# Performance work log

Measured on AMD Instinct MI355X. Metric: run time of the kernel, lower is better.

The kernel has to match this reference:

```python
import jax, jax.numpy as jnp
import numpy as np

B, T, D, H, C, M = 128, 96, 256, 256, 8, 64
COMB = 4 * D + H  # z, z_prime, x_i, global_dynamics, h


def setup_inputs() -> dict:
    key = jax.random.key(0)
    ks = jax.random.split(key, 24)
    X = jax.random.normal(ks[0], (B, T, D), jnp.float32)
    X_last = jax.random.normal(ks[1], (B, T, D), jnp.float32)
    Mask = jax.random.bernoulli(ks[2], 0.5, (B, T, D)).astype(jnp.float32)
    Delta = jax.random.uniform(ks[3], (B, T, D), jnp.float32, 0.0, 5.0)
    X_last_b = jax.random.normal(ks[4], (B, T, D), jnp.float32)
    Delta_b = jax.random.uniform(ks[5], (B, T, D), jnp.float32, 0.0, 5.0)
    x = jnp.stack([X, X_last, Mask, Delta, X_last_b, Delta_b], axis=1)  # [B,6,T,D]
    X_mean = jax.random.normal(ks[6], (1, T, D), jnp.float32)
    clusters = jax.random.randint(ks[7], (D,), 1, C + 1, jnp.int64)
    s = 1.0 / np.sqrt(COMB)
    def U(k, shape, sc):
        return jax.random.uniform(k, shape, jnp.float32, -sc, sc)
    params = {
        'W_i': U(ks[8], (H, COMB), s), 'b_i': U(ks[9], (H,), s),
        'W_f': U(ks[10], (H, COMB), s), 'b_f': U(ks[11], (H,), s),
        'W_o': U(ks[12], (H, COMB), s), 'b_o': U(ks[13], (H,), s),
        'W_c': U(ks[14], (H, COMB), s), 'b_c': U(ks[15], (H,), s),
        'W_fc': U(ks[16], (D, H), 1.0 / np.sqrt(H)), 'b_fc': U(ks[17], (D,), 1.0 / np.sqrt(H)),
        'gz_w': U(ks[18], (D,), 1.0 / np.sqrt(D)), 'gz_b': U(ks[19], (D,), 1.0 / np.sqrt(D)),
        'gzp_w': U(ks[20], (D,), 1.0 / np.sqrt(D)), 'gzp_b': U(ks[21], (D,), 1.0 / np.sqrt(D)),
        'memory': jax.random.uniform(ks[22], (C, M, D), jnp.float32, -1.0 / np.sqrt(M), 1.0 / np.sqrt(M)),
    }
    k2 = jax.random.split(ks[23], 2)
    params['local_w'] = jax.random.uniform(k2[0], (3, D), jnp.float32, -1.0 / np.sqrt(3.0), 1.0 / np.sqrt(3.0))
    params['global_w'] = jax.random.uniform(k2[1], (C,), jnp.float32, -1.0 / np.sqrt(C), 1.0 / np.sqrt(C))
    return dict(x=x, X_mean=X_mean, clusters=clusters, **params)


def reference(x, X_mean, clusters, W_i, b_i, W_f, b_f, W_o, b_o, W_c, b_c,
              W_fc, b_fc, gz_w, gz_b, gzp_w, gzp_b, memory, local_w, global_w):
    # cluster one-hot feature masks: [C, D] (cluster ids are 1-based)
    cmask = (clusters[None, :] == jnp.arange(1, C + 1, dtype=clusters.dtype)[:, None]).astype(x.dtype)

    X, X_last, Mask, Delta, X_last_b, Delta_b = [x[:, i] for i in range(6)]  # each [B,T,D]
    xm = X_mean[0]  # [T,D]

    def step(carry, inp):
        h, c = carry
        xt, xl, xlb, m, d, db, mean = inp
        # FilterLinear with eye filter == diagonal linear; GRU-D decay
        dz = jnp.exp(-jax.nn.relu(d * gz_w + gz_b))
        dzp = jnp.exp(-jax.nn.relu(db * gzp_w + gzp_b))
        z = m * xt + (1 - m) * (dz * xl + (1 - dz) * mean)
        zp = m * xt + (1 - m) * (dzp * xlb + (1 - dzp) * mean)
        x_i = h @ W_fc.T + b_fc  # [B,D]
        local_stats = local_w[0] * z + local_w[1] * zp + local_w[2] * x_i  # [B,D]
        # per-cluster masked local stats -> memory attention
        li = local_stats[:, None, :] * cmask[None]              # [B,C,D]
        scores = jnp.einsum('cmd,bcd->bcm', memory, li)          # [B,C,M]
        s = jax.nn.softmax(scores, axis=-1)
        gd = jnp.einsum('bcm,cmd->bcd', s, memory)               # [B,C,D]
        gd = jnp.einsum('bcd,c->bd', gd, global_w)               # [B,D]
        combined = jnp.concatenate([z, zp, x_i, gd, h], axis=1)  # [B,4D+H]
        i = jax.nn.sigmoid(combined @ W_i.T + b_i)
        f = jax.nn.sigmoid(combined @ W_f.T + b_f)
        o = jax.nn.sigmoid(combined @ W_o.T + b_o)
        ct = jnp.tanh(combined @ W_c.T + b_c)
        c = f * c + i * ct
        h = o * jnp.tanh(c)
        out = h @ W_fc.T + b_fc
        return (h, c), out

    h0 = jnp.zeros((x.shape[0], H), x.dtype)
    c0 = jnp.zeros((x.shape[0], H), x.dtype)
    xs = (X.transpose(1, 0, 2), X_last.transpose(1, 0, 2), X_last_b.transpose(1, 0, 2),
          Mask.transpose(1, 0, 2), Delta.transpose(1, 0, 2), Delta_b.transpose(1, 0, 2), xm)
    _, outs = jax.lax.scan(step, (h0, c0), xs)
    return outs.transpose(1, 0, 2)  # [B,T,D]
```

## Files before the change

### kernel.cpp

```cpp
#include <hip/hip_runtime.h>
#include <hip/hip_bf16.h>
#include <hip/hip_fp16.h>
#include <cstdint>
#include <cstddef>


#define PLANE 24576

using bf16_t = __hip_bfloat16;
typedef __bf16 bf16x8 __attribute__((ext_vector_type(8)));
typedef float  f32x4  __attribute__((ext_vector_type(4)));
typedef unsigned int u32x4 __attribute__((ext_vector_type(4)));

__device__ __forceinline__ float  b2f(bf16_t v){ return __bfloat162float(v); }
__device__ __forceinline__ bf16_t f2b(float v){ return __float2bfloat16(v); }
__device__ __forceinline__ float ldF(const void* p, size_t i, int f32){
  return f32 ? ((const float*)p)[i] : b2f(((const bf16_t*)p)[i]);
}
__device__ __forceinline__ bf16x8 ld_frag(const void* p){
  union { uint4 u; bf16x8 v; } c;
  c.u = *(const uint4*)p;
  return c.v;
}
__device__ __forceinline__ f32x4 mfma_bf16(bf16x8 a, bf16x8 b, f32x4 c){
  return __builtin_amdgcn_mfma_f32_16x16x32_bf16(a, b, c, 0, 0, 0);
}

__device__ __forceinline__ u32x4 ld_cg(const void* p){
  u32x4 r;
  asm volatile("global_load_dwordx4 %0, %1, off sc0 sc1"
               : "=v"(r) : "v"(p) : "memory");
  return r;
}
__device__ __forceinline__ void st_cg(void* p, u32x4 v){
  asm volatile("global_store_dwordx4 %0, %1, off sc0 sc1"
               :: "v"(p), "v"(v) : "memory");
}
__device__ __forceinline__ void st_flag(int* p, int v){
  asm volatile("global_store_dword %0, %1, off sc0 sc1"
               :: "v"(p), "v"(v) : "memory");
}
__device__ __forceinline__ int ld_flag(const int* p){
  int r;
  asm volatile("global_load_dword %0, %1, off sc0 sc1\n\ts_waitcnt vmcnt(0)"
               : "=v"(r) : "v"(p) : "memory");
  return r;
}
__device__ __forceinline__ void vm_wait0(){
  asm volatile("s_waitcnt vmcnt(0)" ::: "memory");
  __builtin_amdgcn_sched_barrier(0);
}

__global__ __launch_bounds__(64) void k_detect(
    const uint32_t* __restrict__ xu, const uint32_t* __restrict__ clu,
    int* __restrict__ flags)
{
  __shared__ int cnt[2];
  int t = threadIdx.x;
  if (t < 2) cnt[t] = 0;
  __syncthreads();
  uint32_t v = xu[2*PLANE + t];
  if (v == 0u || v == 0x3F800000u) atomicAdd(&cnt[0], 1);
  if (clu[2*t + 1] == 0u) atomicAdd(&cnt[1], 1);
  __syncthreads();
  if (t == 0){
    flags[0] = (cnt[0] >= 48) ? 1 : 0;
    flags[1] = (cnt[1] >= 60) ? 1 : 0;
  }
}

__global__ __launch_bounds__(256) void k_zero(int* __restrict__ bar){
  bar[blockIdx.x*256 + threadIdx.x] = 0;
}

__global__ __launch_bounds__(256) void k_canon(
    const void* __restrict__ Wfc, const void* __restrict__ Xmean,
    const void* __restrict__ bfc, const void* __restrict__ localw,
    const void* __restrict__ globalw, const void* __restrict__ gzw,
    const void* __restrict__ gzb, const void* __restrict__ gzpw,
    const void* __restrict__ gzpb, const int* __restrict__ flags,
    bf16_t* __restrict__ WfcC, bf16_t* __restrict__ XmC,
    bf16_t* __restrict__ bfcC, bf16_t* __restrict__ lwC,
    bf16_t* __restrict__ gwC, float* __restrict__ gzC)
{
  const int f32 = flags[0];
  int i = blockIdx.x*256 + threadIdx.x;
  if (i < 65536) WfcC[i] = f2b(ldF(Wfc, i, f32));
  if (i < 24576) XmC[i]  = f2b(ldF(Xmean, i, f32));
  if (i < 256)   bfcC[i] = f2b(ldF(bfc, i, f32));
  if (i < 768)   lwC[i]  = f2b(ldF(localw, i, f32));
  if (i < 8)     gwC[i]  = f2b(ldF(globalw, i, f32));
  if (i < 256){
    gzC[i]       = ldF(gzw,  i, f32);
    gzC[256 + i] = ldF(gzb,  i, f32);
    gzC[512 + i] = ldF(gzpw, i, f32);
    gzC[768 + i] = ldF(gzpb, i, f32);
  }
}

__global__ __launch_bounds__(256) void k_fold(
    const void* __restrict__ Wi, const void* __restrict__ Wf,
    const void* __restrict__ Wo, const void* __restrict__ Wc,
    const void* __restrict__ bi, const void* __restrict__ bfg,
    const void* __restrict__ bo, const void* __restrict__ bcg,
    const void* __restrict__ Wfc, const void* __restrict__ bfc,
    const int* __restrict__ flags,
    bf16_t* __restrict__ U, bf16_t* __restrict__ Uz, float* __restrict__ bias2)
{
  const int f32 = flags[0];
  int n = blockIdx.x; int g = n & 3; int j = n >> 2;
  const void* Wg = (g==0)?Wi:(g==1)?Wf:(g==2)?Wo:Wc;
  const void* bg = (g==0)?bi:(g==1)?bfg:(g==2)?bo:bcg;
  const size_t wb = (size_t)j*1280;
  int k = threadIdx.x;
  float acc = 0.f;
  for (int d=0; d<256; ++d)
    acc += ldF(Wg, wb+512+d, f32) * ldF(Wfc, (size_t)d*256+k, f32);
  U[(size_t)n*512 + k]        = f2b(acc + ldF(Wg, wb+1024+k, f32));
  U[(size_t)n*512 + 256 + k]  = f2b(ldF(Wg, wb+768+k, f32));
  Uz[(size_t)n*512 + k]       = f2b(ldF(Wg, wb+k, f32));
  Uz[(size_t)n*512 + 256 + k] = f2b(ldF(Wg, wb+256+k, f32));
  __shared__ float red[256];
  red[k] = ldF(Wg, wb+512+k, f32) * ldF(bfc, k, f32);
  __syncthreads();
  for (int s=128; s>0; s>>=1){ if (k<s) red[k]+=red[k+s]; __syncthreads(); }
  if (k==0) bias2[n] = red[0] + ldF(bg, j, f32);
}

__global__ __launch_bounds__(256) void k_foldG(
    const void* __restrict__ Wi, const void* __restrict__ Wf,
    const void* __restrict__ Wo, const void* __restrict__ Wc,
    const void* __restrict__ memory, const int* __restrict__ flags,
    bf16_t* __restrict__ G)
{
  const int f32 = flags[0];
  __shared__ float wrow[4][256];
  int j = blockIdx.x; int tid = threadIdx.x;
  const void* Wg[4] = {Wi,Wf,Wo,Wc};
  for (int g=0; g<4; ++g)
    wrow[g][tid] = ldF(Wg[g], (size_t)j*1280 + 768 + tid, f32);
  __syncthreads();
  for (int half=0; half<2; ++half){
    int cm = half*256 + tid;
    float a0=0,a1=0,a2=0,a3=0;
    for (int d=0; d<256; ++d){
      float mv = ldF(memory, (size_t)cm*256 + d, f32);
      a0 += wrow[0][d]*mv; a1 += wrow[1][d]*mv;
      a2 += wrow[2][d]*mv; a3 += wrow[3][d]*mv;
    }
    G[(size_t)(4*j+0)*512 + cm] = f2b(a0);
    G[(size_t)(4*j+1)*512 + cm] = f2b(a1);
    G[(size_t)(4*j+2)*512 + cm] = f2b(a2);
    G[(size_t)(4*j+3)*512 + cm] = f2b(a3);
  }
}

__global__ __launch_bounds__(256) void k_foldQ(
    const int* __restrict__ clusters, const void* __restrict__ memory,
    const bf16_t* __restrict__ lwC, const bf16_t* __restrict__ WfcC,
    const bf16_t* __restrict__ bfcC, const int* __restrict__ flags,
    bf16_t* __restrict__ Mem2, bf16_t* __restrict__ Qbf, float* __restrict__ qb)
{
  const int f32 = flags[0], i64 = flags[1];
  const int cm = blockIdx.x; const int c = cm >> 6;
  const int tid = threadIdx.x;
  __shared__ float ml2[256];
  __shared__ float red[256];
  int cv = i64 ? clusters[2*tid] : clusters[tid];
  float mv = (cv == c+1) ? ldF(memory, (size_t)cm*256 + tid, f32) : 0.f;
  Mem2[(size_t)cm*256 + tid] = f2b(mv);
  float m2 = mv * b2f(lwC[512 + tid]);
  ml2[tid] = m2;
  red[tid] = m2 * b2f(bfcC[tid]);
  __syncthreads();
  float acc = 0.f;
  for (int d=0; d<256; ++d)
    acc += ml2[d] * b2f(WfcC[(size_t)d*256 + tid]);
  Qbf[(size_t)cm*256 + tid] = f2b(acc);
  for (int s=128; s>0; s>>=1){ if (tid<s) red[tid]+=red[tid+s]; __syncthreads(); }
  if (tid==0) qb[cm] = red[0];
}

__global__ __launch_bounds__(256) void k_zzp(
    const void* __restrict__ x, const bf16_t* __restrict__ XmC,
    const float* __restrict__ gzC, const bf16_t* __restrict__ lwC,
    const int* __restrict__ flags,
    bf16_t* __restrict__ Zcat, bf16_t* __restrict__ Zl)
{
  const int f32 = flags[0];
  int r = blockIdx.x;
  int t = r >> 7, b = r & 127, d = threadIdx.x;
  size_t base = (size_t)b*6*PLANE + (size_t)t*256 + d;
  float xt = ldF(x, base          , f32);
  float xl = ldF(x, base +   PLANE, f32);
  float mk = ldF(x, base + 2*PLANE, f32);
  float de = ldF(x, base + 3*PLANE, f32);
  float xlb= ldF(x, base + 4*PLANE, f32);
  float deb= ldF(x, base + 5*PLANE, f32);
  float mean = b2f(XmC[t*256+d]);
  float dz  = expf(-fmaxf(0.f, de *gzC[d]     + gzC[256+d]));
  float dzp = expf(-fmaxf(0.f, deb*gzC[512+d] + gzC[768+d]));
  float z  = mk*xt + (1.f-mk)*(dz *xl  + (1.f-dz )*mean);
  float zp = mk*xt + (1.f-mk)*(dzp*xlb + (1.f-dzp)*mean);
  Zcat[(size_t)r*512 + d]       = f2b(z);
  Zcat[(size_t)r*512 + 256 + d] = f2b(zp);
  Zl[(size_t)r*256 + d] = f2b(b2f(lwC[d])*z + b2f(lwC[256+d])*zp);
}

__global__ __launch_bounds__(256) void k_zc(
    const bf16_t* __restrict__ Zcat, const bf16_t* __restrict__ Uz,
    const float* __restrict__ bias2, __half* __restrict__ zc)
{
  const int tid = threadIdx.x;
  const int w = tid>>6, l = tid&63, q=l>>4, cl=l&15;
  const int mq = w&1, nq = w>>1;
  const int m0 = blockIdx.x*128, n0 = blockIdx.y*128;
  f32x4 acc[4][4];
#pragma unroll
  for (int a=0;a<4;++a)
#pragma unroll
    for (int b2=0;b2<4;++b2) acc[a][b2] = (f32x4){0.f,0.f,0.f,0.f};
  for (int ks=0; ks<16; ++ks){
    bf16x8 av[4], bv[4];
#pragma unroll
    for (int mi=0;mi<4;++mi)
      av[mi] = ld_frag(&Zcat[(size_t)(m0+mq*64+mi*16+cl)*512 + ks*32 + q*8]);
#pragma unroll
    for (int ni=0;ni<4;++ni)
      bv[ni] = ld_frag(&Uz[(size_t)(n0+nq*64+ni*16+cl)*512 + ks*32 + q*8]);
#pragma unroll
    for (int mi=0;mi<4;++mi)
#pragma unroll
      for (int ni=0;ni<4;++ni)
        acc[mi][ni] = mfma_bf16(av[mi], bv[ni], acc[mi][ni]);
  }
#pragma unroll
  for (int mi=0;mi<4;++mi)
#pragma unroll
    for (int ni=0;ni<4;++ni)
#pragma unroll
      for (int rr=0;rr<4;++rr){
        int m = m0 + mq*64 + mi*16 + q*4 + rr;
        int n = n0 + nq*64 + ni*16 + cl;
        zc[(size_t)m*1024 + n] = __float2half(acc[mi][ni][rr] + bias2[n]);
      }
}

__global__ __launch_bounds__(256) void k_szm(
    const bf16_t* __restrict__ Zl, const bf16_t* __restrict__ Mem2,
    const float* __restrict__ qb, __half* __restrict__ SzM)
{
  const int tid = threadIdx.x;
  const int w = tid>>6, l = tid&63, q=l>>4, cl=l&15;
  const int mq = w&1, nq = w>>1;
  const int m0 = blockIdx.x*128, n0 = blockIdx.y*128;
  f32x4 acc[4][4];
#pragma unroll
  for (int a=0;a<4;++a)
#pragma unroll
    for (int b2=0;b2<4;++b2) acc[a][b2] = (f32x4){0.f,0.f,0.f,0.f};
  for (int ks=0; ks<8; ++ks){
    bf16x8 av[4], bv[4];
#pragma unroll
    for (int mi=0;mi<4;++mi)
      av[mi] = ld_frag(&Zl[(size_t)(m0+mq*64+mi*16+cl)*256 + ks*32 + q*8]);
#pragma unroll
    for (int ni=0;ni<4;++ni)
      bv[ni] = ld_frag(&Mem2[(size_t)(n0+nq*64+ni*16+cl)*256 + ks*32 + q*8]);
#pragma unroll
    for (int mi=0;mi<4;++mi)
#pragma unroll
      for (int ni=0;ni<4;++ni)
        acc[mi][ni] = mfma_bf16(av[mi], bv[ni], acc[mi][ni]);
  }
#pragma unroll
  for (int mi=0;mi<4;++mi)
#pragma unroll
    for (int ni=0;ni<4;++ni)
#pragma unroll
      for (int rr=0;rr<4;++rr){
        int m = m0 + mq*64 + mi*16 + q*4 + rr;
        int n = n0 + nq*64 + ni*16 + cl;
        SzM[(size_t)m*512 + n] = __float2half(acc[mi][ni][rr] + qb[n]);
      }
}

__global__ __launch_bounds__(256) void k_out(
    const bf16_t* __restrict__ hSeq, const bf16_t* __restrict__ WfcC,
    const bf16_t* __restrict__ bfcC, const int* __restrict__ flags,
    void* __restrict__ outv)
{
  const int f32 = flags[0];
  const int tid = threadIdx.x;
  const int w = tid>>6, l = tid&63, q=l>>4, cl=l&15;
  const int mq = w&1, nq = w>>1;
  const int m0 = blockIdx.x*128, n0 = blockIdx.y*128;
  f32x4 acc[4][4];
#pragma unroll
  for (int a=0;a<4;++a)
#pragma unroll
    for (int b2=0;b2<4;++b2) acc[a][b2] = (f32x4){0.f,0.f,0.f,0.f};
  for (int ks=0; ks<8; ++ks){
    bf16x8 av[4], bv[4];
#pragma unroll
    for (int mi=0;mi<4;++mi)
      av[mi] = ld_frag(&hSeq[(size_t)(128 + m0+mq*64+mi*16+cl)*256 + ks*32 + q*8]);
#pragma unroll
    for (int ni=0;ni<4;++ni)
      bv[ni] = ld_frag(&WfcC[(size_t)(n0+nq*64+ni*16+cl)*256 + ks*32 + q*8]);
#pragma unroll
    for (int mi=0;mi<4;++mi)
#pragma unroll
      for (int ni=0;ni<4;++ni)
        acc[mi][ni] = mfma_bf16(av[mi], bv[ni], acc[mi][ni]);
  }
#pragma unroll
  for (int mi=0;mi<4;++mi)
#pragma unroll
    for (int ni=0;ni<4;++ni)
#pragma unroll
      for (int rr=0;rr<4;++rr){
        int m = m0 + mq*64 + mi*16 + q*4 + rr;
        int n = n0 + nq*64 + ni*16 + cl;
        float v = acc[mi][ni][rr] + b2f(bfcC[n]);
        int b = m & 127, tt = m >> 7;
        size_t ob = ((size_t)b*96 + tt)*256 + n;
        if (f32) ((float*)outv)[ob] = v; else ((bf16_t*)outv)[ob] = f2b(v);
      }
}

__global__ __launch_bounds__(256) void k_main(
    const bf16_t* __restrict__ gwC,
    const bf16_t* __restrict__ U, const bf16_t* __restrict__ G,
    const bf16_t* __restrict__ Qbf,
    const __half* __restrict__ zc, const __half* __restrict__ SzM,
    bf16_t* __restrict__ hSeq, bf16_t* __restrict__ tSeq,
    int* __restrict__ bar)
{
  __shared__ bf16_t Us[64][264];
  __shared__ bf16_t Gs[64][520];
  __shared__ bf16_t Qs[64][264];
  __shared__ bf16_t hS[16][264];
  __shared__ bf16_t tS[16][520];
  __shared__ bf16_t tO[16][64];
  __shared__ bf16_t hO[16][16];

  const int tid = threadIdx.x;
  const int W = tid>>6, l = tid&63, q = l>>4, cl = l&15;
  const int g = blockIdx.x & 7, s = blockIdx.x >> 3;
  const int r0 = g*16;
  const int n0 = s*64;
  int* barA = bar + g*64;
  int* barB = bar + g*64 + 32;

  for (int i=tid; i<64*32; i+=256){ int r=i>>5, c8=(i&31)*8;
    *(uint4*)(&Us[r][c8]) = *(const uint4*)(U + (size_t)(n0+r)*512 + c8); }
  for (int i=tid; i<64*64; i+=256){ int r=i>>6, c8=(i&63)*8;
    *(uint4*)(&Gs[r][c8]) = *(const uint4*)(G + (size_t)(n0+r)*512 + c8); }
  if (s<8)
    for (int i=tid; i<64*32; i+=256){ int r=i>>5, c8=(i&31)*8;
      *(uint4*)(&Qs[r][c8]) = *(const uint4*)(Qbf + (size_t)(s*64+r)*256 + c8); }
  const float gw_c = (s<8)? b2f(gwC[s]) : 0.f;
  const bool sc_wave = (s<8) && (W==0);
  float creg[4] = {0.f,0.f,0.f,0.f};
  __syncthreads();

  for (int t=0; t<96; ++t){
    f32x4 acc;
#pragma unroll
    for (int rr=0; rr<4; ++rr)
      acc[rr] = __half2float(zc[((size_t)(t*128)+r0+q*4+rr)*1024 + n0 + W*16 + cl]);
    f32x4 sa[4];
    if (sc_wave){
#pragma unroll
      for (int nt=0; nt<4; ++nt)
#pragma unroll
        for (int rr=0; rr<4; ++rr)
          sa[nt][rr] = __half2float(
            SzM[((size_t)(t*128)+r0+q*4+rr)*512 + s*64 + nt*16 + cl]);
    }
    if (W==0){
      if (t>0){
        const int* fp = barA + (l&15);
        int v;
        do { int f = ld_flag(fp); v = (l<16)? f : 0x7fffffff; } while (__any(v < t));
        const bf16_t* hsrc = hSeq + (size_t)t*128*256 + (size_t)r0*256;
        u32x4 hv[8];
#pragma unroll
        for (int k=0;k<8;++k){ int c=l+64*k;
          hv[k] = ld_cg(hsrc + (size_t)(c>>5)*256 + (c&31)*8); }
        vm_wait0();
#pragma unroll
        for (int k=0;k<8;++k){ int c=l+64*k;
          *(u32x4*)(&hS[c>>5][(c&31)*8]) = hv[k]; }
      } else {
#pragma unroll
        for (int k=0;k<8;++k){ int c=l+64*k;
          *(u32x4*)(&hS[c>>5][(c&31)*8]) = (u32x4){0,0,0,0}; }
      }
    }
    __syncthreads();
    if (sc_wave){
#pragma unroll
      for (int ks=0; ks<8; ++ks){
        bf16x8 a = ld_frag(&hS[cl][ks*32 + q*8]);
#pragma unroll
        for (int nt=0; nt<4; ++nt)
          sa[nt] = mfma_bf16(a, ld_frag(&Qs[nt*16+cl][ks*32 + q*8]), sa[nt]);
      }
#pragma unroll
      for (int rr=0; rr<4; ++rr){
        float mx = fmaxf(fmaxf(sa[0][rr],sa[1][rr]), fmaxf(sa[2][rr],sa[3][rr]));
        mx = fmaxf(mx, __shfl_xor(mx,1));
        mx = fmaxf(mx, __shfl_xor(mx,2));
        mx = fmaxf(mx, __shfl_xor(mx,4));
        mx = fmaxf(mx, __shfl_xor(mx,8));
        float e0=expf(sa[0][rr]-mx), e1=expf(sa[1][rr]-mx);
        float e2=expf(sa[2][rr]-mx), e3=expf(sa[3][rr]-mx);
        float sm = e0+e1+e2+e3;
        sm += __shfl_xor(sm,1); sm += __shfl_xor(sm,2);
        sm += __shfl_xor(sm,4); sm += __shfl_xor(sm,8);
        float sc = gw_c/sm;
        tO[q*4+rr][ 0+cl] = f2b(e0*sc);
        tO[q*4+rr][16+cl] = f2b(e1*sc);
        tO[q*4+rr][32+cl] = f2b(e2*sc);
        tO[q*4+rr][48+cl] = f2b(e3*sc);
      }
      bf16_t* tdst = tSeq + (size_t)t*128*512 + (size_t)r0*512 + s*64;
#pragma unroll
      for (int k=0;k<2;++k){ int c=l+64*k;
        u32x4 v = *(u32x4*)(&tO[c>>3][(c&7)*8]);
        st_cg(tdst + (size_t)(c>>3)*512 + (c&7)*8, v); }
      vm_wait0();
      if (l==0) st_flag(barB + s, t+1);
    }
#pragma unroll
    for (int ks=0; ks<8; ++ks)
      acc = mfma_bf16(ld_frag(&hS[cl][ks*32 + q*8]),
                      ld_frag(&Us[W*16+cl][ks*32 + q*8]), acc);
    if (W==1){
      const int* fp = barB + (l&7);
      int v;
      do { int f = ld_flag(fp); v = (l<8)? f : 0x7fffffff; } while (__any(v < t+1));
      const bf16_t* tsrc = tSeq + (size_t)t*128*512 + (size_t)r0*512;
      u32x4 tv[16];
#pragma unroll
      for (int k=0;k<16;++k){ int c=l+64*k;
        tv[k] = ld_cg(tsrc + (size_t)(c>>6)*512 + (c&63)*8); }
      vm_wait0();
#pragma unroll
      for (int k=0;k<16;++k){ int c=l+64*k;
        *(u32x4*)(&tS[c>>6][(c&63)*8]) = tv[k]; }
    }
    __syncthreads();
#pragma unroll
    for (int ks=0; ks<16; ++ks)
      acc = mfma_bf16(ld_frag(&tS[cl][ks*32 + q*8]),
                      ld_frag(&Gs[W*16+cl][ks*32 + q*8]), acc);
    const int base = l & ~3;
#pragma unroll
    for (int rr=0; rr<4; ++rr){
      float p = acc[rr];
      float pi = __shfl(p, base+0);
      float pf = __shfl(p, base+1);
      float po = __shfl(p, base+2);
      float pc = __shfl(p, base+3);
      float iv = 1.f/(1.f+expf(-pi));
      float fv = 1.f/(1.f+expf(-pf));
      float ov = 1.f/(1.f+expf(-po));
      float cv = tanhf(pc);
      float cn = fv*creg[rr] + iv*cv;
      creg[rr] = cn;
      float hv = ov * tanhf(cn);
      if ((l&3)==0)
        hO[q*4+rr][W*4 + (cl>>2)] = f2b(hv);
    }
    __syncthreads();
    if (W==0){
      if (l < 32){
        u32x4 v = *(u32x4*)(&hO[l>>1][(l&1)*8]);
        st_cg(hSeq + (size_t)(t+1)*128*256 + (size_t)(r0+(l>>1))*256
                   + s*16 + (l&1)*8, v);
      }
      vm_wait0();
      if (l==0) st_flag(barA + s, t+1);
    }
  }
}

extern "C" void kernel_launch(void* const* d_in, const int* in_sizes, int n_in,
                              void* d_out, int out_size, void* d_ws, size_t ws_size,
                              hipStream_t stream)
{
  const void* x       = d_in[0];
  const void* Xmean   = d_in[1];
  const int*  clusters= (const int*)d_in[2];
  const void* Wi  = d_in[3];
  const void* bi  = d_in[4];
  const void* Wf  = d_in[5];
  const void* bfp = d_in[6];
  const void* Wo  = d_in[7];
  const void* bo  = d_in[8];
  const void* Wc  = d_in[9];
  const void* bcp = d_in[10];
  const void* Wfc = d_in[11];
  const void* bfc = d_in[12];
  const void* gzw = d_in[13];
  const void* gzb = d_in[14];
  const void* gzpw= d_in[15];
  const void* gzpb= d_in[16];
  const void* memory = d_in[17];
  const void* localw = d_in[18];
  const void* globalw= d_in[19];
  (void)in_sizes; (void)n_in; (void)out_size; (void)ws_size;

  char* ws = (char*)d_ws;
  size_t off = 0;
  auto take = [&](size_t bytes)->char*{
    char* p = ws + off; off = (off + bytes + 255) & ~(size_t)255; return p; };
  int*    flags  = (int*)   take(16);
  int*    bar    = (int*)   take(512*4);
  bf16_t* U      = (bf16_t*)take((size_t)1024*512*2);
  bf16_t* Uz     = (bf16_t*)take((size_t)1024*512*2);
  bf16_t* G      = (bf16_t*)take((size_t)1024*512*2);
  bf16_t* WfcC   = (bf16_t*)take((size_t)65536*2);
  bf16_t* XmC    = (bf16_t*)take((size_t)24576*2);
  bf16_t* bfcC   = (bf16_t*)take(256*2);
  bf16_t* lwC    = (bf16_t*)take(768*2);
  bf16_t* gwC    = (bf16_t*)take(8*2);
  float*  gzC    = (float*) take(1024*4);
  float*  bias2  = (float*) take(1024*4);
  bf16_t* Mem2   = (bf16_t*)take((size_t)512*256*2);
  bf16_t* Qbf    = (bf16_t*)take((size_t)512*256*2);
  float*  qb     = (float*) take(512*4);
  __half* zc     = (__half*)take((size_t)12288*1024*2);
  __half* SzM    = (__half*)take((size_t)12288*512*2);
  char* bigA = take((size_t)12288*512*2);
  char* bigB = take((size_t)97*128*256*2);
  bf16_t* Zcat = (bf16_t*)bigA;
  bf16_t* tSeq = (bf16_t*)bigA;
  bf16_t* Zl   = (bf16_t*)bigB;
  bf16_t* hSeq = (bf16_t*)bigB;

  k_detect<<<1,    64, 0,stream>>>((const uint32_t*)x, (const uint32_t*)clusters, flags);
  k_zero  <<<2,    256,0,stream>>>(bar);
  k_canon <<<256,  256,0,stream>>>(Wfc, Xmean, bfc, localw, globalw,
                                   gzw, gzb, gzpw, gzpb, flags,
                                   WfcC, XmC, bfcC, lwC, gwC, gzC);
  k_fold  <<<1024, 256,0,stream>>>(Wi,Wf,Wo,Wc, bi,bfp,bo,bcp, Wfc,bfc, flags,
                                   U, Uz, bias2);
  k_foldG <<<256,  256,0,stream>>>(Wi,Wf,Wo,Wc, memory, flags, G);
  k_foldQ <<<512,  256,0,stream>>>(clusters, memory, lwC, WfcC, bfcC, flags,
                                   Mem2, Qbf, qb);
  k_zzp   <<<12288,256,0,stream>>>(x, XmC, gzC, lwC, flags, Zcat, Zl);
  k_zc    <<<dim3(96,8),256,0,stream>>>(Zcat, Uz, bias2, zc);
  k_szm   <<<dim3(96,4),256,0,stream>>>(Zl, Mem2, qb, SzM);
  k_main  <<<128,  256,0,stream>>>(gwC, U, G, Qbf, zc, SzM, hSeq, tSeq, bar);
  k_out   <<<dim3(96,2),256,0,stream>>>(hSeq, WfcC, bfcC, flags, d_out);
}
```

Measured before the change: 1.077 ms.

## Merge prep kernels and compute attention softmax redundantly per block

Folds the zero-barrier kernel into k_canon and merges the four fold/zzp prep kernels into a single k_prep dispatch. The two GEMM kernels are combined into k_pre2, which cuts the number of launches. In k_main, every wave now computes memory-attention scores for all 8 clusters locally, reading Qbf straight from global memory. This drops the tSeq global exchange and the second cross-block flag barrier (barB), at the cost of redundant MFMA and softmax work per block and more global loads of Qbf on each step.

```diff
diff --git a/kernel.cpp b/kernel.cpp
--- a/kernel.cpp
+++ b/kernel.cpp
@@ -69,10 +69,6 @@
   }
 }
 
-__global__ __launch_bounds__(256) void k_zero(int* __restrict__ bar){
-  bar[blockIdx.x*256 + threadIdx.x] = 0;
-}
-
 __global__ __launch_bounds__(256) void k_canon(
     const void* __restrict__ Wfc, const void* __restrict__ Xmean,
     const void* __restrict__ bfc, const void* __restrict__ localw,
@@ -81,10 +77,12 @@
     const void* __restrict__ gzpb, const int* __restrict__ flags,
     bf16_t* __restrict__ WfcC, bf16_t* __restrict__ XmC,
     bf16_t* __restrict__ bfcC, bf16_t* __restrict__ lwC,
-    bf16_t* __restrict__ gwC, float* __restrict__ gzC)
+    bf16_t* __restrict__ gwC, float* __restrict__ gzC,
+    int* __restrict__ bar)
 {
   const int f32 = flags[0];
   int i = blockIdx.x*256 + threadIdx.x;
+  if (blockIdx.x < 4) bar[i] = 0;
   if (i < 65536) WfcC[i] = f2b(ldF(Wfc, i, f32));
   if (i < 24576) XmC[i]  = f2b(ldF(Xmean, i, f32));
   if (i < 256)   bfcC[i] = f2b(ldF(bfc, i, f32));
@@ -98,191 +96,169 @@
   }
 }
 
-__global__ __launch_bounds__(256) void k_fold(
+__global__ __launch_bounds__(256) void k_prep(
     const void* __restrict__ Wi, const void* __restrict__ Wf,
     const void* __restrict__ Wo, const void* __restrict__ Wc,
     const void* __restrict__ bi, const void* __restrict__ bfg,
     const void* __restrict__ bo, const void* __restrict__ bcg,
     const void* __restrict__ Wfc, const void* __restrict__ bfc,
-    const int* __restrict__ flags,
-    bf16_t* __restrict__ U, bf16_t* __restrict__ Uz, float* __restrict__ bias2)
-{
-  const int f32 = flags[0];
-  int n = blockIdx.x; int g = n & 3; int j = n >> 2;
-  const void* Wg = (g==0)?Wi:(g==1)?Wf:(g==2)?Wo:Wc;
-  const void* bg = (g==0)?bi:(g==1)?bfg:(g==2)?bo:bcg;
-  const size_t wb = (size_t)j*1280;
-  int k = threadIdx.x;
-  float acc = 0.f;
-  for (int d=0; d<256; ++d)
-    acc += ldF(Wg, wb+512+d, f32) * ldF(Wfc, (size_t)d*256+k, f32);
-  U[(size_t)n*512 + k]        = f2b(acc + ldF(Wg, wb+1024+k, f32));
-  U[(size_t)n*512 + 256 + k]  = f2b(ldF(Wg, wb+768+k, f32));
-  Uz[(size_t)n*512 + k]       = f2b(ldF(Wg, wb+k, f32));
-  Uz[(size_t)n*512 + 256 + k] = f2b(ldF(Wg, wb+256+k, f32));
-  __shared__ float red[256];
-  red[k] = ldF(Wg, wb+512+k, f32) * ldF(bfc, k, f32);
-  __syncthreads();
-  for (int s=128; s>0; s>>=1){ if (k<s) red[k]+=red[k+s]; __syncthreads(); }
-  if (k==0) bias2[n] = red[0] + ldF(bg, j, f32);
-}
-
-__global__ __launch_bounds__(256) void k_foldG(
-    const void* __restrict__ Wi, const void* __restrict__ Wf,
-    const void* __restrict__ Wo, const void* __restrict__ Wc,
-    const void* __restrict__ memory, const int* __restrict__ flags,
-    bf16_t* __restrict__ G)
-{
-  const int f32 = flags[0];
-  __shared__ float wrow[4][256];
-  int j = blockIdx.x; int tid = threadIdx.x;
-  const void* Wg[4] = {Wi,Wf,Wo,Wc};
-  for (int g=0; g<4; ++g)
-    wrow[g][tid] = ldF(Wg[g], (size_t)j*1280 + 768 + tid, f32);
-  __syncthreads();
-  for (int half=0; half<2; ++half){
-    int cm = half*256 + tid;
-    float a0=0,a1=0,a2=0,a3=0;
-    for (int d=0; d<256; ++d){
-      float mv = ldF(memory, (size_t)cm*256 + d, f32);
-      a0 += wrow[0][d]*mv; a1 += wrow[1][d]*mv;
-      a2 += wrow[2][d]*mv; a3 += wrow[3][d]*mv;
-    }
-    G[(size_t)(4*j+0)*512 + cm] = f2b(a0);
-    G[(size_t)(4*j+1)*512 + cm] = f2b(a1);
-    G[(size_t)(4*j+2)*512 + cm] = f2b(a2);
-    G[(size_t)(4*j+3)*512 + cm] = f2b(a3);
-  }
-}
-
-__global__ __launch_bounds__(256) void k_foldQ(
-    const int* __restrict__ clusters, const void* __restrict__ memory,
+    const void* __restrict__ memory, const int* __restrict__ clusters,
+    const void* __restrict__ x,
+    const bf16_t* __restrict__ XmC, const float* __restrict__ gzC,
     const bf16_t* __restrict__ lwC, const bf16_t* __restrict__ WfcC,
     const bf16_t* __restrict__ bfcC, const int* __restrict__ flags,
-    bf16_t* __restrict__ Mem2, bf16_t* __restrict__ Qbf, float* __restrict__ qb)
-{
+    bf16_t* __restrict__ U, bf16_t* __restrict__ Uz,
+    float* __restrict__ bias2, bf16_t* __restrict__ G,
+    bf16_t* __restrict__ Mem2, bf16_t* __restrict__ Qbf,
+    float* __restrict__ qb,
+    bf16_t* __restrict__ Zcat, bf16_t* __restrict__ Zl)
+{
+  __shared__ float sA[4][256];
+  __shared__ float red[256];
   const int f32 = flags[0], i64 = flags[1];
-  const int cm = blockIdx.x; const int c = cm >> 6;
-  const int tid = threadIdx.x;
-  __shared__ float ml2[256];
-  __shared__ float red[256];
-  int cv = i64 ? clusters[2*tid] : clusters[tid];
-  float mv = (cv == c+1) ? ldF(memory, (size_t)cm*256 + tid, f32) : 0.f;
-  Mem2[(size_t)cm*256 + tid] = f2b(mv);
-  float m2 = mv * b2f(lwC[512 + tid]);
-  ml2[tid] = m2;
-  red[tid] = m2 * b2f(bfcC[tid]);
-  __syncthreads();
-  float acc = 0.f;
-  for (int d=0; d<256; ++d)
-    acc += ml2[d] * b2f(WfcC[(size_t)d*256 + tid]);
-  Qbf[(size_t)cm*256 + tid] = f2b(acc);
-  for (int s=128; s>0; s>>=1){ if (tid<s) red[tid]+=red[tid+s]; __syncthreads(); }
-  if (tid==0) qb[cm] = red[0];
-}
-
-__global__ __launch_bounds__(256) void k_zzp(
-    const void* __restrict__ x, const bf16_t* __restrict__ XmC,
-    const float* __restrict__ gzC, const bf16_t* __restrict__ lwC,
-    const int* __restrict__ flags,
-    bf16_t* __restrict__ Zcat, bf16_t* __restrict__ Zl)
-{
-  const int f32 = flags[0];
-  int r = blockIdx.x;
-  int t = r >> 7, b = r & 127, d = threadIdx.x;
-  size_t base = (size_t)b*6*PLANE + (size_t)t*256 + d;
-  float xt = ldF(x, base          , f32);
-  float xl = ldF(x, base +   PLANE, f32);
-  float mk = ldF(x, base + 2*PLANE, f32);
-  float de = ldF(x, base + 3*PLANE, f32);
-  float xlb= ldF(x, base + 4*PLANE, f32);
-  float deb= ldF(x, base + 5*PLANE, f32);
-  float mean = b2f(XmC[t*256+d]);
-  float dz  = expf(-fmaxf(0.f, de *gzC[d]     + gzC[256+d]));
-  float dzp = expf(-fmaxf(0.f, deb*gzC[512+d] + gzC[768+d]));
-  float z  = mk*xt + (1.f-mk)*(dz *xl  + (1.f-dz )*mean);
-  float zp = mk*xt + (1.f-mk)*(dzp*xlb + (1.f-dzp)*mean);
-  Zcat[(size_t)r*512 + d]       = f2b(z);
-  Zcat[(size_t)r*512 + 256 + d] = f2b(zp);
-  Zl[(size_t)r*256 + d] = f2b(b2f(lwC[d])*z + b2f(lwC[256+d])*zp);
-}
-
-__global__ __launch_bounds__(256) void k_zc(
+  const int bid = blockIdx.x, tid = threadIdx.x;
+
+  if (bid < 1024){
+    int n = bid; int g = n & 3; int j = n >> 2;
+    const void* Wg = (g==0)?Wi:(g==1)?Wf:(g==2)?Wo:Wc;
+    const void* bg = (g==0)?bi:(g==1)?bfg:(g==2)?bo:bcg;
+    const size_t wb = (size_t)j*1280;
+    int k = tid;
+    float acc = 0.f;
+    for (int d=0; d<256; ++d)
+      acc += ldF(Wg, wb+512+d, f32) * ldF(Wfc, (size_t)d*256+k, f32);
+    U[(size_t)n*512 + k]        = f2b(acc + ldF(Wg, wb+1024+k, f32));
+    U[(size_t)n*512 + 256 + k]  = f2b(ldF(Wg, wb+768+k, f32));
+    Uz[(size_t)n*512 + k]       = f2b(ldF(Wg, wb+k, f32));
+    Uz[(size_t)n*512 + 256 + k] = f2b(ldF(Wg, wb+256+k, f32));
+    red[k] = ldF(Wg, wb+512+k, f32) * ldF(bfc, k, f32);
+    __syncthreads();
+    for (int s=128; s>0; s>>=1){ if (k<s) red[k]+=red[k+s]; __syncthreads(); }
+    if (k==0) bias2[n] = red[0] + ldF(bg, j, f32);
+  } else if (bid < 1280){
+    int j = bid - 1024;
+    const void* Wg[4] = {Wi,Wf,Wo,Wc};
+    for (int g=0; g<4; ++g)
+      sA[g][tid] = ldF(Wg[g], (size_t)j*1280 + 768 + tid, f32);
+    __syncthreads();
+    for (int half=0; half<2; ++half){
+      int cm = half*256 + tid;
+      float a0=0,a1=0,a2=0,a3=0;
+      for (int d=0; d<256; ++d){
+        float mv = ldF(memory, (size_t)cm*256 + d, f32);
+        a0 += sA[0][d]*mv; a1 += sA[1][d]*mv;
+        a2 += sA[2][d]*mv; a3 += sA[3][d]*mv;
+      }
+      G[(size_t)(4*j+0)*512 + cm] = f2b(a0);
+      G[(size_t)(4*j+1)*512 + cm] = f2b(a1);
+      G[(size_t)(4*j+2)*512 + cm] = f2b(a2);
+      G[(size_t)(4*j+3)*512 + cm] = f2b(a3);
+    }
+  } else if (bid < 1792){
+    const int cm = bid - 1280; const int c = cm >> 6;
+    int cv = i64 ? clusters[2*tid] : clusters[tid];
+    float mv = (cv == c+1) ? ldF(memory, (size_t)cm*256 + tid, f32) : 0.f;
+    Mem2[(size_t)cm*256 + tid] = f2b(mv);
+    float m2 = mv * b2f(lwC[512 + tid]);
+    sA[0][tid] = m2;
+    red[tid] = m2 * b2f(bfcC[tid]);
+    __syncthreads();
+    float acc = 0.f;
+    for (int d=0; d<256; ++d)
+      acc += sA[0][d] * b2f(WfcC[(size_t)d*256 + tid]);
+    Qbf[(size_t)cm*256 + tid] = f2b(acc);
+    for (int s=128; s>0; s>>=1){ if (tid<s) red[tid]+=red[tid+s]; __syncthreads(); }
+    if (tid==0) qb[cm] = red[0];
+  } else {
+    int r = bid - 1792;
+    int t = r >> 7, b = r & 127, d = tid;
+    size_t base = (size_t)b*6*PLANE + (size_t)t*256 + d;
+    float xt = ldF(x, base          , f32);
+    float xl = ldF(x, base +   PLANE, f32);
+    float mk = ldF(x, base + 2*PLANE, f32);
+    float de = ldF(x, base + 3*PLANE, f32);
+    float xlb= ldF(x, base + 4*PLANE, f32);
+    float deb= ldF(x, base + 5*PLANE, f32);
+    float mean = b2f(XmC[t*256+d]);
+    float dz  = expf(-fmaxf(0.f, de *gzC[d]     + gzC[256+d]));
+    float dzp = expf(-fmaxf(0.f, deb*gzC[512+d] + gzC[768+d]));
+    float z  = mk*xt + (1.f-mk)*(dz *xl  + (1.f-dz )*mean);
+    float zp = mk*xt + (1.f-mk)*(dzp*xlb + (1.f-dzp)*mean);
+    Zcat[(size_t)r*512 + d]       = f2b(z);
+    Zcat[(size_t)r*512 + 256 + d] = f2b(zp);
+    Zl[(size_t)r*256 + d] = f2b(b2f(lwC[d])*z + b2f(lwC[256+d])*zp);
+  }
+}
+
+__global__ __launch_bounds__(256) void k_pre2(
     const bf16_t* __restrict__ Zcat, const bf16_t* __restrict__ Uz,
-    const float* __restrict__ bias2, __half* __restrict__ zc)
+    const float* __restrict__ bias2,
+    const bf16_t* __restrict__ Zl, const bf16_t* __restrict__ Mem2,
+    const float* __restrict__ qb,
+    __half* __restrict__ zc, __half* __restrict__ SzM)
 {
   const int tid = threadIdx.x;
   const int w = tid>>6, l = tid&63, q=l>>4, cl=l&15;
   const int mq = w&1, nq = w>>1;
-  const int m0 = blockIdx.x*128, n0 = blockIdx.y*128;
+  const int m0 = blockIdx.x*128;
   f32x4 acc[4][4];
 #pragma unroll
   for (int a=0;a<4;++a)
 #pragma unroll
     for (int b2=0;b2<4;++b2) acc[a][b2] = (f32x4){0.f,0.f,0.f,0.f};
-  for (int ks=0; ks<16; ++ks){
-    bf16x8 av[4], bv[4];
+  if (blockIdx.y < 8){
+    const int n0 = blockIdx.y*128;
+    for (int ks=0; ks<16; ++ks){
+      bf16x8 av[4], bv[4];
+#pragma unroll
+      for (int mi=0;mi<4;++mi)
+        av[mi] = ld_frag(&Zcat[(size_t)(m0+mq*64+mi*16+cl)*512 + ks*32 + q*8]);
+#pragma unroll
+      for (int ni=0;ni<4;++ni)
+        bv[ni] = ld_frag(&Uz[(size_t)(n0+nq*64+ni*16+cl)*512 + ks*32 + q*8]);
+#pragma unroll
+      for (int mi=0;mi<4;++mi)
+#pragma unroll
+        for (int ni=0;ni<4;++ni)
+          acc[mi][ni] = mfma_bf16(av[mi], bv[ni], acc[mi][ni]);
+    }
 #pragma unroll
     for (int mi=0;mi<4;++mi)
-      av[mi] = ld_frag(&Zcat[(size_t)(m0+mq*64+mi*16+cl)*512 + ks*32 + q*8]);
-#pragma unroll
-    for (int ni=0;ni<4;++ni)
-      bv[ni] = ld_frag(&Uz[(size_t)(n0+nq*64+ni*16+cl)*512 + ks*32 + q*8]);
+#pragma unroll
+      for (int ni=0;ni<4;++ni)
+#pragma unroll
+        for (int rr=0;rr<4;++rr){
+          int m = m0 + mq*64 + mi*16 + q*4 + rr;
+          int n = n0 + nq*64 + ni*16 + cl;
+          zc[(size_t)m*1024 + n] = __float2half(acc[mi][ni][rr] + bias2[n]);
+        }
+  } else {
+    const int n0 = (blockIdx.y-8)*128;
+    for (int ks=0; ks<8; ++ks){
+      bf16x8 av[4], bv[4];
+#pragma unroll
+      for (int mi=0;mi<4;++mi)
+        av[mi] = ld_frag(&Zl[(size_t)(m0+mq*64+mi*16+cl)*256 + ks*32 + q*8]);
+#pragma unroll
+      for (int ni=0;ni<4;++ni)
+        bv[ni] = ld_frag(&Mem2[(size_t)(n0+nq*64+ni*16+cl)*256 + ks*32 + q*8]);
+#pragma unroll
+      for (int mi=0;mi<4;++mi)
+#pragma unroll
+        for (int ni=0;ni<4;++ni)
+          acc[mi][ni] = mfma_bf16(av[mi], bv[ni], acc[mi][ni]);
+    }
 #pragma unroll
     for (int mi=0;mi<4;++mi)
 #pragma unroll
       for (int ni=0;ni<4;++ni)
-        acc[mi][ni] = mfma_bf16(av[mi], bv[ni], acc[mi][ni]);
+#pragma unroll
+        for (int rr=0;rr<4;++rr){
+          int m = m0 + mq*64 + mi*16 + q*4 + rr;
+          int n = n0 + nq*64 + ni*16 + cl;
+          SzM[(size_t)m*512 + n] = __float2half(acc[mi][ni][rr] + qb[n]);
+        }
   }
-#pragma unroll
-  for (int mi=0;mi<4;++mi)
-#pragma unroll
-    for (int ni=0;ni<4;++ni)
-#pragma unroll
-      for (int rr=0;rr<4;++rr){
-        int m = m0 + mq*64 + mi*16 + q*4 + rr;
-        int n = n0 + nq*64 + ni*16 + cl;
-        zc[(size_t)m*1024 + n] = __float2half(acc[mi][ni][rr] + bias2[n]);
-      }
-}
-
-__global__ __launch_bounds__(256) void k_szm(
-    const bf16_t* __restrict__ Zl, const bf16_t* __restrict__ Mem2,
-    const float* __restrict__ qb, __half* __restrict__ SzM)
-{
-  const int tid = threadIdx.x;
-  const int w = tid>>6, l = tid&63, q=l>>4, cl=l&15;
-  const int mq = w&1, nq = w>>1;
-  const int m0 = blockIdx.x*128, n0 = blockIdx.y*128;
-  f32x4 acc[4][4];
-#pragma unroll
-  for (int a=0;a<4;++a)
-#pragma unroll
-    for (int b2=0;b2<4;++b2) acc[a][b2] = (f32x4){0.f,0.f,0.f,0.f};
-  for (int ks=0; ks<8; ++ks){
-    bf16x8 av[4], bv[4];
-#pragma unroll
-    for (int mi=0;mi<4;++mi)
-      av[mi] = ld_frag(&Zl[(size_t)(m0+mq*64+mi*16+cl)*256 + ks*32 + q*8]);
-#pragma unroll
-    for (int ni=0;ni<4;++ni)
-      bv[ni] = ld_frag(&Mem2[(size_t)(n0+nq*64+ni*16+cl)*256 + ks*32 + q*8]);
-#pragma unroll
-    for (int mi=0;mi<4;++mi)
-#pragma unroll
-      for (int ni=0;ni<4;++ni)
-        acc[mi][ni] = mfma_bf16(av[mi], bv[ni], acc[mi][ni]);
-  }
-#pragma unroll
-  for (int mi=0;mi<4;++mi)
-#pragma unroll
-    for (int ni=0;ni<4;++ni)
-#pragma unroll
-      for (int rr=0;rr<4;++rr){
-        int m = m0 + mq*64 + mi*16 + q*4 + rr;
-        int n = n0 + nq*64 + ni*16 + cl;
-        SzM[(size_t)m*512 + n] = __float2half(acc[mi][ni][rr] + qb[n]);
-      }
 }
 
 __global__ __launch_bounds__(256) void k_out(
@@ -334,15 +310,12 @@
     const bf16_t* __restrict__ U, const bf16_t* __restrict__ G,
     const bf16_t* __restrict__ Qbf,
     const __half* __restrict__ zc, const __half* __restrict__ SzM,
-    bf16_t* __restrict__ hSeq, bf16_t* __restrict__ tSeq,
-    int* __restrict__ bar)
-{
-  __shared__ bf16_t Us[64][264];
-  __shared__ bf16_t Gs[64][520];
-  __shared__ bf16_t Qs[64][264];
-  __shared__ bf16_t hS[16][264];
-  __shared__ bf16_t tS[16][520];
-  __shared__ bf16_t tO[16][64];
+    bf16_t* __restrict__ hSeq, int* __restrict__ bar)
+{
+  __shared__ bf16_t Us[64][260];
+  __shared__ bf16_t Gs[64][516];
+  __shared__ bf16_t hS[16][260];
+  __shared__ bf16_t tT[16][516];
   __shared__ bf16_t hO[16][16];
 
   const int tid = threadIdx.x;
@@ -351,17 +324,13 @@
   const int r0 = g*16;
   const int n0 = s*64;
   int* barA = bar + g*64;
-  int* barB = bar + g*64 + 32;
 
   for (int i=tid; i<64*32; i+=256){ int r=i>>5, c8=(i&31)*8;
     *(uint4*)(&Us[r][c8]) = *(const uint4*)(U + (size_t)(n0+r)*512 + c8); }
   for (int i=tid; i<64*64; i+=256){ int r=i>>6, c8=(i&63)*8;
     *(uint4*)(&Gs[r][c8]) = *(const uint4*)(G + (size_t)(n0+r)*512 + c8); }
-  if (s<8)
-    for (int i=tid; i<64*32; i+=256){ int r=i>>5, c8=(i&31)*8;
-      *(uint4*)(&Qs[r][c8]) = *(const uint4*)(Qbf + (size_t)(s*64+r)*256 + c8); }
-  const float gw_c = (s<8)? b2f(gwC[s]) : 0.f;
-  const bool sc_wave = (s<8) && (W==0);
+  const float gw0 = b2f(gwC[2*W]);
+  const float gw1 = b2f(gwC[2*W+1]);
   float creg[4] = {0.f,0.f,0.f,0.f};
   __syncthreads();
 
@@ -370,15 +339,13 @@
 #pragma unroll
     for (int rr=0; rr<4; ++rr)
       acc[rr] = __half2float(zc[((size_t)(t*128)+r0+q*4+rr)*1024 + n0 + W*16 + cl]);
-    f32x4 sa[4];
-    if (sc_wave){
-#pragma unroll
-      for (int nt=0; nt<4; ++nt)
-#pragma unroll
-        for (int rr=0; rr<4; ++rr)
-          sa[nt][rr] = __half2float(
-            SzM[((size_t)(t*128)+r0+q*4+rr)*512 + s*64 + nt*16 + cl]);
-    }
+    f32x4 sa[8];
+#pragma unroll
+    for (int nt=0; nt<8; ++nt)
+#pragma unroll
+      for (int rr=0; rr<4; ++rr)
+        sa[nt][rr] = __half2float(
+          SzM[((size_t)(t*128)+r0+q*4+rr)*512 + W*128 + nt*16 + cl]);
     if (W==0){
       if (t>0){
         const int* fp = barA + (l&15);
@@ -400,62 +367,47 @@
       }
     }
     __syncthreads();
-    if (sc_wave){
-#pragma unroll
-      for (int ks=0; ks<8; ++ks){
-        bf16x8 a = ld_frag(&hS[cl][ks*32 + q*8]);
-#pragma unroll
-        for (int nt=0; nt<4; ++nt)
-          sa[nt] = mfma_bf16(a, ld_frag(&Qs[nt*16+cl][ks*32 + q*8]), sa[nt]);
-      }
+    const bf16_t* Qb = Qbf + (size_t)(W*128)*256;
+#pragma unroll
+    for (int ks=0; ks<8; ++ks){
+      bf16x8 a = ld_frag(&hS[cl][ks*32 + q*8]);
+#pragma unroll
+      for (int nt=0; nt<8; ++nt)
+        sa[nt] = mfma_bf16(a,
+          ld_frag(Qb + (size_t)(nt*16+cl)*256 + ks*32 + q*8), sa[nt]);
+    }
+#pragma unroll
+    for (int ks=0; ks<8; ++ks)
+      acc = mfma_bf16(ld_frag(&hS[cl][ks*32 + q*8]),
+                      ld_frag(&Us[W*16+cl][ks*32 + q*8]), acc);
+#pragma unroll
+    for (int half=0; half<2; ++half){
+      const float gw = half ? gw1 : gw0;
+      const int o = half*4;
 #pragma unroll
       for (int rr=0; rr<4; ++rr){
-        float mx = fmaxf(fmaxf(sa[0][rr],sa[1][rr]), fmaxf(sa[2][rr],sa[3][rr]));
+        float mx = fmaxf(fmaxf(sa[o][rr],sa[o+1][rr]),
+                         fmaxf(sa[o+2][rr],sa[o+3][rr]));
         mx = fmaxf(mx, __shfl_xor(mx,1));
         mx = fmaxf(mx, __shfl_xor(mx,2));
         mx = fmaxf(mx, __shfl_xor(mx,4));
         mx = fmaxf(mx, __shfl_xor(mx,8));
-        float e0=expf(sa[0][rr]-mx), e1=expf(sa[1][rr]-mx);
-        float e2=expf(sa[2][rr]-mx), e3=expf(sa[3][rr]-mx);
+        float e0=expf(sa[o  ][rr]-mx), e1=expf(sa[o+1][rr]-mx);
+        float e2=expf(sa[o+2][rr]-mx), e3=expf(sa[o+3][rr]-mx);
         float sm = e0+e1+e2+e3;
         sm += __shfl_xor(sm,1); sm += __shfl_xor(sm,2);
         sm += __shfl_xor(sm,4); sm += __shfl_xor(sm,8);
-        float sc = gw_c/sm;
-        tO[q*4+rr][ 0+cl] = f2b(e0*sc);
-        tO[q*4+rr][16+cl] = f2b(e1*sc);
-        tO[q*4+rr][32+cl] = f2b(e2*sc);
-        tO[q*4+rr][48+cl] = f2b(e3*sc);
+        float sc = gw/sm;
+        tT[q*4+rr][W*128 + (o  )*16 + cl] = f2b(e0*sc);
+        tT[q*4+rr][W*128 + (o+1)*16 + cl] = f2b(e1*sc);
+        tT[q*4+rr][W*128 + (o+2)*16 + cl] = f2b(e2*sc);
+        tT[q*4+rr][W*128 + (o+3)*16 + cl] = f2b(e3*sc);
       }
-      bf16_t* tdst = tSeq + (size_t)t*128*512 + (size_t)r0*512 + s*64;
-#pragma unroll
-      for (int k=0;k<2;++k){ int c=l+64*k;
-        u32x4 v = *(u32x4*)(&tO[c>>3][(c&7)*8]);
-        st_cg(tdst + (size_t)(c>>3)*512 + (c&7)*8, v); }
-      vm_wait0();
-      if (l==0) st_flag(barB + s, t+1);
-    }
-#pragma unroll
-    for (int ks=0; ks<8; ++ks)
-      acc = mfma_bf16(ld_frag(&hS[cl][ks*32 + q*8]),
-                      ld_frag(&Us[W*16+cl][ks*32 + q*8]), acc);
-    if (W==1){
-      const int* fp = barB + (l&7);
-      int v;
-      do { int f = ld_flag(fp); v = (l<8)? f : 0x7fffffff; } while (__any(v < t+1));
-      const bf16_t* tsrc = tSeq + (size_t)t*128*512 + (size_t)r0*512;
-      u32x4 tv[16];
-#pragma unroll
-      for (int k=0;k<16;++k){ int c=l+64*k;
-        tv[k] = ld_cg(tsrc + (size_t)(c>>6)*512 + (c&63)*8); }
-      vm_wait0();
-#pragma unroll
-      for (int k=0;k<16;++k){ int c=l+64*k;
-        *(u32x4*)(&tS[c>>6][(c&63)*8]) = tv[k]; }
     }
     __syncthreads();
 #pragma unroll
     for (int ks=0; ks<16; ++ks)
-      acc = mfma_bf16(ld_frag(&tS[cl][ks*32 + q*8]),
+      acc = mfma_bf16(ld_frag(&tT[cl][ks*32 + q*8]),
                       ld_frag(&Gs[W*16+cl][ks*32 + q*8]), acc);
     const int base = l & ~3;
 #pragma unroll
@@ -519,7 +471,7 @@
   auto take = [&](size_t bytes)->char*{
     char* p = ws + off; off = (off + bytes + 255) & ~(size_t)255; return p; };
   int*    flags  = (int*)   take(16);
-  int*    bar    = (int*)   take(512*4);
+  int*    bar    = (int*)   take(1024*4);
   bf16_t* U      = (bf16_t*)take((size_t)1024*512*2);
   bf16_t* Uz     = (bf16_t*)take((size_t)1024*512*2);
   bf16_t* G      = (bf16_t*)take((size_t)1024*512*2);
@@ -535,26 +487,19 @@
   float*  qb     = (float*) take(512*4);
   __half* zc     = (__half*)take((size_t)12288*1024*2);
   __half* SzM    = (__half*)take((size_t)12288*512*2);
-  char* bigA = take((size_t)12288*512*2);
-  char* bigB = take((size_t)97*128*256*2);
-  bf16_t* Zcat = (bf16_t*)bigA;
-  bf16_t* tSeq = (bf16_t*)bigA;
-  bf16_t* Zl   = (bf16_t*)bigB;
-  bf16_t* hSeq = (bf16_t*)bigB;
+  bf16_t* Zcat   = (bf16_t*)take((size_t)12288*512*2);
+  bf16_t* Zl     = (bf16_t*)take((size_t)12288*256*2);
+  bf16_t* hSeq   = (bf16_t*)take((size_t)97*128*256*2);
 
   k_detect<<<1,    64, 0,stream>>>((const uint32_t*)x, (const uint32_t*)clusters, flags);
-  k_zero  <<<2,    256,0,stream>>>(bar);
   k_canon <<<256,  256,0,stream>>>(Wfc, Xmean, bfc, localw, globalw,
                                    gzw, gzb, gzpw, gzpb, flags,
-                                   WfcC, XmC, bfcC, lwC, gwC, gzC);
-  k_fold  <<<1024, 256,0,stream>>>(Wi,Wf,Wo,Wc, bi,bfp,bo,bcp, Wfc,bfc, flags,
-                                   U, Uz, bias2);
-  k_foldG <<<256,  256,0,stream>>>(Wi,Wf,Wo,Wc, memory, flags, G);
-  k_foldQ <<<512,  256,0,stream>>>(clusters, memory, lwC, WfcC, bfcC, flags,
-                                   Mem2, Qbf, qb);
-  k_zzp   <<<12288,256,0,stream>>>(x, XmC, gzC, lwC, flags, Zcat, Zl);
-  k_zc    <<<dim3(96,8),256,0,stream>>>(Zcat, Uz, bias2, zc);
-  k_szm   <<<dim3(96,4),256,0,stream>>>(Zl, Mem2, qb, SzM);
-  k_main  <<<128,  256,0,stream>>>(gwC, U, G, Qbf, zc, SzM, hSeq, tSeq, bar);
+                                   WfcC, XmC, bfcC, lwC, gwC, gzC, bar);
+  k_prep  <<<14080,256,0,stream>>>(Wi,Wf,Wo,Wc, bi,bfp,bo,bcp, Wfc,bfc,
+                                   memory, clusters, x,
+                                   XmC, gzC, lwC, WfcC, bfcC, flags,
+                                   U, Uz, bias2, G, Mem2, Qbf, qb, Zcat, Zl);
+  k_pre2  <<<dim3(96,12),256,0,stream>>>(Zcat, Uz, bias2, Zl, Mem2, qb, zc, SzM);
+  k_main  <<<128,  256,0,stream>>>(gwC, U, G, Qbf, zc, SzM, hSeq, bar);
   k_out   <<<dim3(96,2),256,0,stream>>>(hSeq, WfcC, bfcC, flags, d_out);
 }
```

Result: slower. 2.166 ms (+101.2%).
